# Optimization experiments

Hardware: AMD Instinct MI355X
Metric: run time of the kernel (lower is better)

## Reference

```python
import jax, jax.numpy as jnp
import numpy as np

D_MODEL = 1024
NHEAD = 16
HEAD_DIM = D_MODEL // NHEAD
EPS = 1e-8


def setup_inputs() -> dict:
    key = jax.random.key(0)
    ks = jax.random.split(key, 10)
    B, T = 2, 2048
    s = 1.0 / np.sqrt(D_MODEL)
    return {
        "query": jax.random.normal(ks[0], (B, T, D_MODEL), jnp.float32),
        "key": jax.random.normal(ks[1], (B, T, D_MODEL), jnp.float32),
        "value": jax.random.normal(ks[2], (B, T, D_MODEL), jnp.float32),
        "frac": jax.random.uniform(ks[3], (B, T), jnp.float32),
        "Wq": jax.random.normal(ks[4], (D_MODEL, D_MODEL), jnp.float32) * s,
        "bq": jnp.zeros((D_MODEL,), jnp.float32),
        "Wk": jax.random.normal(ks[5], (D_MODEL, D_MODEL), jnp.float32) * s,
        "bk": jnp.zeros((D_MODEL,), jnp.float32),
        "Wv": jax.random.normal(ks[6], (D_MODEL, D_MODEL), jnp.float32) * s,
        "bv": jnp.zeros((D_MODEL,), jnp.float32),
        "attn_bias": jax.random.normal(ks[7], (HEAD_DIM,), jnp.float32) * 0.02,
        "Wo": jax.random.normal(ks[8], (D_MODEL, D_MODEL), jnp.float32) * s,
        "bo": jnpp if False else jnp.zeros((D_MODEL,), jnp.float32),
    }


def reference(query, key, value, frac, Wq, bq, Wk, bk, Wv, bv, attn_bias, Wo, bo):
    B, T, _ = query.shape
    H, Dh = NHEAD, HEAD_DIM
    scale = Dh ** -0.5

    # torch Linear: x @ W.T + b
    Q = (query @ Wq.T + bq).reshape(B, T, H, Dh).transpose(0, 2, 1, 3)  # [B,H,T,Dh]
    K = (key @ Wk.T + bk).reshape(B, T, H, Dh).transpose(0, 2, 1, 3)
    V = (value @ Wv.T + bv).reshape(B, T, H, Dh).transpose(0, 2, 1, 3)

    # factor_ij = (frac_j - frac_i) / (frac_i*frac_j + eps), shape [B,T,T]
    fi = frac[:, :, None]
    fj = frac[:, None, :]
    factor = (fj - fi) / (fi * fj + EPS)

    # sum_d (Q_i*K_j + attn_bias*factor)_d == QK^T + sum(attn_bias)*factor
    bias_sum = jnp.sum(attn_bias)
    logits = jnp.einsum('bhid,bhjd->bhij', Q, K) + bias_sum * factor[:, None, :, :]
    logits = logits * scale

    probs = jax.nn.softmax(logits, axis=-1)  # dropout p=0.0 (eval)
    out = jnp.einsum('bhij,bhjd->bhid', probs, V)  # [B,H,T,Dh]
    out = out.transpose(0, 2, 1, 3).reshape(B, T, H * Dh)
    return out @ Wo.T + bo
```

## Files before the change

kernel.cpp:

```cpp
#include <hip/hip_runtime.h>

typedef short s16x8 __attribute__((ext_vector_type(8)));
typedef float f32x4 __attribute__((ext_vector_type(4)));
typedef unsigned int u32x2 __attribute__((ext_vector_type(2)));
typedef unsigned short u16;
typedef unsigned int u32;

#define D_MODEL 1024
#define NHEAD   16
#define HD      64
#define TSEQ    2048
#define NB      2
#define MROWS   4096
#define NSPLIT  2
#define NTILES  (TSEQ / 64 / NSPLIT)

#define LOG2E 1.4426950408889634f
#define QSCALE (0.125f * LOG2E)

__device__ __forceinline__ u16 f2bf(float f) {
  unsigned u = __builtin_bit_cast(unsigned, f);
  u += 0x7fffu + ((u >> 16) & 1u);
  return (u16)(u >> 16);
}

__device__ __forceinline__ float bf2f(u16 x) {
  return __builtin_bit_cast(float, (u32)x << 16);
}

__device__ __forceinline__ u32 cvtpk(float lo, float hi) {
  u32 r;
  asm("v_cvt_pk_bf16_f32 %0, %1, %2" : "=v"(r) : "v"(lo), "v"(hi));
  return r;
}

__device__ __forceinline__ float exp2fast(float x) {
#if __has_builtin(__builtin_amdgcn_exp2f)
  return __builtin_amdgcn_exp2f(x);
#else
  return exp2f(x);
#endif
}

__device__ __forceinline__ float rcpfast(float x) {
#if __has_builtin(__builtin_amdgcn_rcpf)
  return __builtin_amdgcn_rcpf(x);
#else
  return 1.f / x;
#endif
}

__device__ __forceinline__ void gload16(const void* g, void* l) {
  __builtin_amdgcn_global_load_lds((const __attribute__((address_space(1))) void*)g,
                                   (__attribute__((address_space(3))) void*)l,
                                   16, 0, 0);
}

__global__ void cvt_all(const float* __restrict__ q, const float* __restrict__ k,
                        const float* __restrict__ v, const float* __restrict__ wq,
                        const float* __restrict__ wk, const float* __restrict__ wv,
                        const float* __restrict__ wo, const float* __restrict__ ab,
                        u16* qb, u16* kb, u16* vb, u16* wqb, u16* wkb, u16* wvb, u16* wob,
                        float* bsum) {
  if (blockIdx.x == 16384) {
    if (threadIdx.x < 64) {
      float s = ab[threadIdx.x];
#pragma unroll
      for (int m = 32; m >= 1; m >>= 1) s += __shfl_xor(s, m);
      if (threadIdx.x == 0) bsum[0] = s * 0.125f * LOG2E;
    }
    return;
  }
  int i = blockIdx.x * 256 + threadIdx.x;
  const float* src; u16* dst; int off;
  if (i < 3 * 1048576) {
    int t = i >> 20; off = i & 1048575;
    src = (t == 0) ? q : (t == 1) ? k : v;
    dst = (t == 0) ? qb : (t == 1) ? kb : vb;
  } else {
    int j = i - 3 * 1048576;
    int t = j >> 18; off = j & 262143;
    src = (t == 0) ? wq : (t == 1) ? wk : (t == 2) ? wv : wo;
    dst = (t == 0) ? wqb : (t == 1) ? wkb : (t == 2) ? wvb : wob;
  }
  float4 x = ((const float4*)src)[off];
  ushort4 o;
  o.x = f2bf(x.x); o.y = f2bf(x.y); o.z = f2bf(x.z); o.w = f2bf(x.w);
  ((ushort4*)dst)[off] = o;
}

template <int BM, int BN, int WN, int MODE>
__device__ __forceinline__ void gemm_core(const u16* __restrict__ A, const u16* __restrict__ Bt,
                                          const float* __restrict__ bias, void* __restrict__ out,
                                          float oscale, u16* lds) {
  constexpr int K = 1024, N = 1024;
  constexpr int WM = 4 / WN;
  constexpr int WTM = BM / WM, WTN = BN / WN;
  constexpr int MR = WTM / 16, NR = WTN / 16;
  constexpr int ASZ = BM * 32, BSZ = BN * 32;
  constexpr int AISS = ASZ / 2048, BISS = BSZ / 2048;
  u16* lA = lds;
  u16* lB = lds + 2 * ASZ;

  const int tid = threadIdx.x;
  const int wid = tid >> 6, lane = tid & 63;
  const int l15 = lane & 15, lgp = lane >> 4;
  const int wr = wid / WN, wc = wid % WN;
  const int m0 = blockIdx.y * BM, n0 = blockIdx.x * BN;

  const u16* gA[AISS];
  const u16* gB[BISS];
#pragma unroll
  for (int i = 0; i < AISS; ++i) {
    int tp = i * 256 + tid, row = tp % BM, kc = tp / BM;
    gA[i] = A + (size_t)(m0 + row) * K + kc * 8;
  }
#pragma unroll
  for (int i = 0; i < BISS; ++i) {
    int tp = i * 256 + tid, row = tp % BN, kc = tp / BN;
    gB[i] = Bt + (size_t)(n0 + row) * K + kc * 8;
  }

  f32x4 acc[MR][NR];
#pragma unroll
  for (int m = 0; m < MR; ++m)
#pragma unroll
    for (int n = 0; n < NR; ++n) acc[m][n] = (f32x4){0.f, 0.f, 0.f, 0.f};

  auto stage = [&](int buf, int k0) {
#pragma unroll
    for (int i = 0; i < AISS; ++i)
      gload16(gA[i] + k0, lA + buf * ASZ + (i * 256 + tid) * 8);
#pragma unroll
    for (int i = 0; i < BISS; ++i)
      gload16(gB[i] + k0, lB + buf * BSZ + (i * 256 + tid) * 8);
  };

  int cur = 0;
  stage(0, 0);
  __syncthreads();
  for (int k0 = 0; k0 < K; k0 += 32) {
    if (k0 + 32 < K) stage(cur ^ 1, k0 + 32);
    const u16* a = lA + cur * ASZ;
    const u16* b = lB + cur * BSZ;
    s16x8 af[MR], bf[NR];
#pragma unroll
    for (int m = 0; m < MR; ++m)
      af[m] = *(const s16x8*)(a + lgp * BM * 8 + (wr * WTM + m * 16 + l15) * 8);
#pragma unroll
    for (int n = 0; n < NR; ++n)
      bf[n] = *(const s16x8*)(b + lgp * BN * 8 + (wc * WTN + n * 16 + l15) * 8);
    __builtin_amdgcn_s_setprio(1);
#pragma unroll
    for (int m = 0; m < MR; ++m)
#pragma unroll
      for (int n = 0; n < NR; ++n) {
        if (MODE == 1)
          acc[m][n] = __builtin_amdgcn_mfma_f32_16x16x32_bf16(bf[n], af[m], acc[m][n], 0, 0, 0);
        else
          acc[m][n] = __builtin_amdgcn_mfma_f32_16x16x32_bf16(af[m], bf[n], acc[m][n], 0, 0, 0);
      }
    __builtin_amdgcn_s_setprio(0);
    __syncthreads();
    cur ^= 1;
  }

  if (MODE == 1) {
    float4 bvv4[NR];
#pragma unroll
    for (int n = 0; n < NR; ++n)
      bvv4[n] = *(const float4*)(bias + n0 + wc * WTN + n * 16 + lgp * 4);
#pragma unroll
    for (int m = 0; m < MR; ++m) {
      int m_abs = m0 + wr * WTM + m * 16 + l15;
      int bb = m_abs >> 11, t = m_abs & 2047;
#pragma unroll
      for (int n = 0; n < NR; ++n) {
#pragma unroll
        for (int r = 0; r < 4; ++r) {
          int n_abs = n0 + wc * WTN + n * 16 + lgp * 4 + r;
          int h = n_abs >> 6, d = n_abs & 63;
          float vv = (acc[m][n][r] + ((const float*)&bvv4[n])[r]) * oscale;
          ((u16*)out)[(((size_t)((bb * NHEAD + h) * HD + d)) << 11) + t] = f2bf(vv);
        }
      }
    }
  } else {
    float bvv[NR];
#pragma unroll
    for (int n = 0; n < NR; ++n) bvv[n] = bias[n0 + wc * WTN + n * 16 + l15];
#pragma unroll
    for (int m = 0; m < MR; ++m) {
      int rowb = m0 + wr * WTM + m * 16 + lgp * 4;
#pragma unroll
      for (int n = 0; n < NR; ++n) {
        int col = n0 + wc * WTN + n * 16 + l15;
#pragma unroll
        for (int r = 0; r < 4; ++r) {
          int row = rowb + r;
          float vv = (acc[m][n][r] + bvv[n]) * oscale;
          if (MODE == 2) {
            ((float*)out)[(size_t)row * N + col] = vv;
          } else {
            int b = row >> 11, t = row & 2047;
            int h = col >> 6, d = col & 63;
            ((u16*)out)[(((size_t)(b * NHEAD + h) * TSEQ + t) << 6) + d] = f2bf(vv);
          }
        }
      }
    }
  }
}

__global__ __launch_bounds__(256) void gemm_qkv(const u16* __restrict__ qb, const u16* __restrict__ kb,
                                                const u16* __restrict__ vb,
                                                const u16* __restrict__ Wqb, const u16* __restrict__ Wkb,
                                                const u16* __restrict__ Wvb,
                                                const float* __restrict__ bq, const float* __restrict__ bk,
                                                const float* __restrict__ bv,
                                                u16* Qp, u16* Kp, u16* Vtp) {
  __shared__ __align__(16) u16 lds[2 * 128 * 32 * 2];
  int z = blockIdx.z;
  if (z == 0)
    gemm_core<128, 128, 2, 0>(qb, Wqb, bq, Qp, QSCALE, lds);
  else if (z == 1)
    gemm_core<128, 128, 2, 0>(kb, Wkb, bk, Kp, 1.0f, lds);
  else
    gemm_core<128, 128, 2, 1>(vb, Wvb, bv, Vtp, 1.0f, lds);
}

__global__ __launch_bounds__(256) void gemm_out(const u16* __restrict__ A, const u16* __restrict__ Bt,
                                                const float* __restrict__ bias, float* __restrict__ out) {
  __shared__ __align__(16) u16 lds[2 * 64 * 32 + 2 * 128 * 32];
  gemm_core<64, 128, 4, 2>(A, Bt, bias, out, 1.0f, lds);
}

__global__ __launch_bounds__(512, 4) void attn_kernel(const u16* __restrict__ Qp,
                                                      const u16* __restrict__ Kp,
                                                      const u16* __restrict__ Vt,
                                                      const float* __restrict__ frac,
                                                      const float* __restrict__ bsum,
                                                      u16* __restrict__ o0,
                                                      u16* __restrict__ o1,
                                                      float2* __restrict__ ml) {
  __shared__ __align__(16) u16 kbuf[64 * 64];
  __shared__ __align__(16) u16 vbuf[2][64 * 64];
  __shared__ __align__(16) u16 plds[8][16 * 64];
  const int tid = threadIdx.x, wid = tid >> 6, lane = tid & 63;
  const int l15 = lane & 15, lgp = lane >> 4;
  const int bh = blockIdx.y, b = bh >> 4, h = bh & 15;
  const int z = blockIdx.z;
  const int kvbase = z * (TSEQ / NSPLIT);
  u16* opart = z ? o1 : o0;
  float2* mlz = ml + z * (NB * NHEAD * TSEQ);
  const u16* Qh = Qp + (size_t)bh * TSEQ * HD;
  const u16* Kh = Kp + (size_t)bh * TSEQ * HD;
  const u16* Vh = Vt + (size_t)bh * HD * TSEQ;
  const float* fb = frac + b * TSEQ;
  const float bs = bsum[0];
  const float THR2 = 24.0f;
  const int q0 = blockIdx.x * 128 + wid * 16;

  const int srow = lane >> 3;
  const int sg8 = ((lane & 7) ^ srow) * 8;
  const int rbase = wid * 8 + srow;

  const int ofs0 = l15 * 64 + ((lgp ^ (l15 & 7)) * 8);
  const int ofs1 = l15 * 64 + (((4 + lgp) ^ (l15 & 7)) * 8);

  s16x8 qf[2];
#pragma unroll
  for (int ks = 0; ks < 2; ++ks)
    qf[ks] = *(const s16x8*)(Qh + (size_t)(q0 + l15) * HD + ks * 32 + lgp * 8);

  const float fi = fb[q0 + l15];
  const float nbfi = -bs * fi;
  float m2run = -1e30f;
  float lsum = 0.f;
  f32x4 o[4];
#pragma unroll
  for (int nd = 0; nd < 4; ++nd) o[nd] = (f32x4){0.f, 0.f, 0.f, 0.f};

  auto stageK = [&](int t) {
    int kv0s = kvbase + t * 64;
    gload16(Kh + (size_t)(kv0s + rbase) * HD + sg8, &kbuf[wid * 512]);
  };
  auto stageV = [&](int buf, int t) {
    int kv0s = kvbase + t * 64;
    gload16(Vh + (size_t)rbase * TSEQ + kv0s + sg8, &vbuf[buf][wid * 512]);
  };

  int cur = 0;
  stageK(0);
  stageV(0, 0);
  __syncthreads();

  for (int t = 0; t < NTILES; ++t) {
    s16x8 kf[4][2];
#pragma unroll
    for (int n = 0; n < 4; ++n) {
      kf[n][0] = *(const s16x8*)(&kbuf[0] + n * 1024 + ofs0);
      kf[n][1] = *(const s16x8*)(&kbuf[0] + n * 1024 + ofs1);
    }
    float4 fj4[4];
#pragma unroll
    for (int n = 0; n < 4; ++n)
      fj4[n] = *(const float4*)(fb + kvbase + t * 64 + n * 16 + lgp * 4);

    __syncthreads();
    if (t + 1 < NTILES) { stageK(t + 1); stageV(cur ^ 1, t + 1); }

    f32x4 s[4];
    __builtin_amdgcn_s_setprio(1);
#pragma unroll
    for (int n = 0; n < 4; ++n) {
      f32x4 a = (f32x4){0.f, 0.f, 0.f, 0.f};
      a = __builtin_amdgcn_mfma_f32_16x16x32_bf16(kf[n][0], qf[0], a, 0, 0, 0);
      a = __builtin_amdgcn_mfma_f32_16x16x32_bf16(kf[n][1], qf[1], a, 0, 0, 0);
      s[n] = a;
    }
    __builtin_amdgcn_s_setprio(0);

    float pmax = -1e30f;
#pragma unroll
    for (int n = 0; n < 4; ++n) {
#pragma unroll
      for (int r = 0; r < 4; ++r) {
        float fj = (r == 0) ? fj4[n].x : (r == 1) ? fj4[n].y : (r == 2) ? fj4[n].z : fj4[n].w;
        float num = __builtin_fmaf(bs, fj, nbfi);
        float den = __builtin_fmaf(fi, fj, 1e-8f);
        float l2 = __builtin_fmaf(num, rcpfast(den), s[n][r]);
        s[n][r] = l2;
        pmax = fmaxf(pmax, l2);
      }
    }

    if (__any((pmax - m2run) > THR2)) {
      float tm = fmaxf(pmax, __shfl_xor(pmax, 16));
      tm = fmaxf(tm, __shfl_xor(tm, 32));
      float m2n = fmaxf(m2run, tm);
      float alpha = exp2fast(m2run - m2n);
      lsum *= alpha;
      m2run = m2n;
      float af[4];
#pragma unroll
      for (int r = 0; r < 4; ++r) af[r] = __shfl(alpha, lgp * 4 + r);
#pragma unroll
      for (int nd = 0; nd < 4; ++nd)
#pragma unroll
        for (int r = 0; r < 4; ++r) o[nd][r] *= af[r];
    }

    u32 w[4][2];
    {
      float ps = 0.f;
#pragma unroll
      for (int n = 0; n < 4; ++n) {
#pragma unroll
        for (int s2 = 0; s2 < 2; ++s2) {
          float p0 = exp2fast(s[n][2 * s2 + 0] - m2run);
          float p1 = exp2fast(s[n][2 * s2 + 1] - m2run);
          ps += p0 + p1;
          w[n][s2] = cvtpk(p0, p1);
        }
      }
      lsum += ps;
    }

    u16* pw = &plds[wid][0];
#pragma unroll
    for (int n = 0; n < 4; ++n) {
      int idx = l15 * 64 + ((n * 16 + lgp * 4) ^ ((l15 & 7) << 3));
      *(u32x2*)(pw + idx) = (u32x2){w[n][0], w[n][1]};
    }
    s16x8 pf[2];
#pragma unroll
    for (int ks = 0; ks < 2; ++ks) {
      int idx = l15 * 64 + ((ks * 32 + lgp * 8) ^ ((l15 & 7) << 3));
      pf[ks] = *(const s16x8*)(pw + idx);
    }

    const u16* vbp = &vbuf[cur][0];
    __builtin_amdgcn_s_setprio(1);
#pragma unroll
    for (int nd = 0; nd < 4; ++nd) {
      s16x8 vf0 = *(const s16x8*)(vbp + nd * 1024 + ofs0);
      s16x8 vf1 = *(const s16x8*)(vbp + nd * 1024 + ofs1);
      o[nd] = __builtin_amdgcn_mfma_f32_16x16x32_bf16(pf[0], vf0, o[nd], 0, 0, 0);
      o[nd] = __builtin_amdgcn_mfma_f32_16x16x32_bf16(pf[1], vf1, o[nd], 0, 0, 0);
    }
    __builtin_amdgcn_s_setprio(0);

    __syncthreads();
    cur ^= 1;
  }

  {
    float l = lsum;
    l += __shfl_xor(l, 16);
    l += __shfl_xor(l, 32);
    if (lgp == 0)
      mlz[(bh << 11) + q0 + l15] = make_float2(m2run, l);
#pragma unroll
    for (int nd = 0; nd < 4; ++nd)
#pragma unroll
      for (int r = 0; r < 4; ++r) {
        int q = q0 + lgp * 4 + r;
        opart[((size_t)(b * TSEQ + q)) * D_MODEL + h * HD + nd * 16 + l15] = f2bf(o[nd][r]);
      }
  }
}

__global__ __launch_bounds__(256) void attn_combine(const u16* __restrict__ o0,
                                                    const u16* __restrict__ o1,
                                                    const float2* __restrict__ ml,
                                                    u16* __restrict__ aout) {
  int g = blockIdx.x * 256 + threadIdx.x;
  int bth = g >> 3, j0 = (g & 7) * 8;
  int b = bth >> 15, t = (bth >> 4) & 2047, h = bth & 15;
  int mlidx = (((b << 4) | h) << 11) | t;
  float2 v0 = ml[mlidx];
  float2 v1 = ml[NB * NHEAD * TSEQ + mlidx];
  float M = fmaxf(v0.x, v1.x);
  float a0 = exp2fast(v0.x - M), a1 = exp2fast(v1.x - M);
  float rd = __fdividef(1.f, __builtin_fmaf(v0.y, a0, v1.y * a1));
  float s0 = a0 * rd, s1 = a1 * rd;
  size_t base = (size_t)bth * 64 + j0;
  s16x8 x0 = *(const s16x8*)(o0 + base);
  s16x8 x1 = *(const s16x8*)(o1 + base);
  s16x8 out;
#pragma unroll
  for (int j = 0; j < 8; ++j) {
    float f = __builtin_fmaf(bf2f((u16)x0[j]), s0, bf2f((u16)x1[j]) * s1);
    out[j] = (short)f2bf(f);
  }
  *(s16x8*)(aout + base) = out;
}

extern "C" void kernel_launch(void* const* d_in, const int* in_sizes, int n_in,
                              void* d_out, int out_size, void* d_ws, size_t ws_size,
                              hipStream_t stream) {
  const float* query = (const float*)d_in[0];
  const float* key_  = (const float*)d_in[1];
  const float* value = (const float*)d_in[2];
  const float* frac  = (const float*)d_in[3];
  const float* Wq    = (const float*)d_in[4];
  const float* bq    = (const float*)d_in[5];
  const float* Wk    = (const float*)d_in[6];
  const float* bk    = (const float*)d_in[7];
  const float* Wv    = (const float*)d_in[8];
  const float* bv    = (const float*)d_in[9];
  const float* abias = (const float*)d_in[10];
  const float* Wo    = (const float*)d_in[11];
  const float* bo    = (const float*)d_in[12];

  char* ws = (char*)d_ws;
  size_t off = 0;
  auto alloc = [&](size_t bytes) { char* p = ws + off; off += (bytes + 255) & ~255ULL; return p; };
  const size_t XB = (size_t)MROWS * D_MODEL * 2;
  const size_t WB = (size_t)D_MODEL * D_MODEL * 2;
  u16* qb  = (u16*)alloc(XB);
  u16* kb  = (u16*)alloc(XB);
  u16* vb  = (u16*)alloc(XB);
  u16* Wqb = (u16*)alloc(WB);
  u16* Wkb = (u16*)alloc(WB);
  u16* Wvb = (u16*)alloc(WB);
  u16* Wob = (u16*)alloc(WB);
  float* bsum = (float*)alloc(256);
  u16* Qp  = (u16*)alloc(XB);
  u16* Kp  = (u16*)alloc(XB);
  u16* Vtp = (u16*)alloc(XB);
  u16* AO  = (u16*)alloc(XB);

  u16* o0 = qb;
  u16* o1 = kb;
  float2* ml = (float2*)vb;

  cvt_all<<<dim3(16385), dim3(256), 0, stream>>>(query, key_, value, Wq, Wk, Wv, Wo, abias,
                                                 qb, kb, vb, Wqb, Wkb, Wvb, Wob, bsum);

  gemm_qkv<<<dim3(D_MODEL / 128, MROWS / 128, 3), dim3(256), 0, stream>>>(
      qb, kb, vb, Wqb, Wkb, Wvb, bq, bk, bv, Qp, Kp, Vtp);

  attn_kernel<<<dim3(TSEQ / 128, NB * NHEAD, NSPLIT), dim3(512), 0, stream>>>(
      Qp, Kp, Vtp, frac, bsum, o0, o1, ml);

  attn_combine<<<dim3(MROWS * D_MODEL / 8 / 256), dim3(256), 0, stream>>>(o0, o1, ml, AO);

  gemm_out<<<dim3(D_MODEL / 128, MROWS / 64), dim3(256), 0, stream>>>(AO, Wob, bo, (float*)d_out);
}
```

Measured before the change: 182.3 us.

## Switch attention to 32x32x16 MFMA with register-only P via permlane32 swap

The attention kernel moves from 16x16x32 to 32x32x16 bf16 MFMA tiles, with each wave owning 32 query rows. The block shrinks from 512 to 256 threads and each thread now stages two K and two V chunks. The softmax probability tile is rearranged into the B-operand layout in registers using v_permlane32_swap instead of a per-wave LDS round trip. The aims are fewer MFMA issues, no P store/load through LDS, and fewer shuffles for the running-max rescale, at the cost of more accumulator registers per lane and halved threads per block.

```diff
diff --git a/kernel.cpp b/kernel.cpp
--- a/kernel.cpp
+++ b/kernel.cpp
@@ -2,7 +2,9 @@
 
 typedef short s16x8 __attribute__((ext_vector_type(8)));
 typedef float f32x4 __attribute__((ext_vector_type(4)));
+typedef float f32x16 __attribute__((ext_vector_type(16)));
 typedef unsigned int u32x2 __attribute__((ext_vector_type(2)));
+typedef unsigned int u32x4 __attribute__((ext_vector_type(4)));
 typedef unsigned short u16;
 typedef unsigned int u32;
 
@@ -235,7 +237,7 @@
   gemm_core<64, 128, 4, 2>(A, Bt, bias, out, 1.0f, lds);
 }
 
-__global__ __launch_bounds__(512, 4) void attn_kernel(const u16* __restrict__ Qp,
+__global__ __launch_bounds__(256, 4) void attn_kernel(const u16* __restrict__ Qp,
                                                       const u16* __restrict__ Kp,
                                                       const u16* __restrict__ Vt,
                                                       const float* __restrict__ frac,
@@ -245,9 +247,9 @@
                                                       float2* __restrict__ ml) {
   __shared__ __align__(16) u16 kbuf[64 * 64];
   __shared__ __align__(16) u16 vbuf[2][64 * 64];
-  __shared__ __align__(16) u16 plds[8][16 * 64];
   const int tid = threadIdx.x, wid = tid >> 6, lane = tid & 63;
-  const int l15 = lane & 15, lgp = lane >> 4;
+  const int l31 = lane & 31, hi = lane >> 5, hi4 = hi * 4, hi8 = hi * 8;
+  const int ksw = l31 & 7;
   const int bh = blockIdx.y, b = bh >> 4, h = bh & 15;
   const int z = blockIdx.z;
   const int kvbase = z * (TSEQ / NSPLIT);
@@ -259,135 +261,129 @@
   const float* fb = frac + b * TSEQ;
   const float bs = bsum[0];
   const float THR2 = 24.0f;
-  const int q0 = blockIdx.x * 128 + wid * 16;
-
-  const int srow = lane >> 3;
-  const int sg8 = ((lane & 7) ^ srow) * 8;
-  const int rbase = wid * 8 + srow;
-
-  const int ofs0 = l15 * 64 + ((lgp ^ (l15 & 7)) * 8);
-  const int ofs1 = l15 * 64 + (((4 + lgp) ^ (l15 & 7)) * 8);
-
-  s16x8 qf[2];
-#pragma unroll
-  for (int ks = 0; ks < 2; ++ks)
-    qf[ks] = *(const s16x8*)(Qh + (size_t)(q0 + l15) * HD + ks * 32 + lgp * 8);
-
-  const float fi = fb[q0 + l15];
+  const int q0w = blockIdx.x * 128 + wid * 32;
+
+  const int r_0 = tid >> 3, c_0 = ((tid & 7) ^ (r_0 & 7)) * 8;
+  const int r_1 = 32 + r_0, c_1 = ((tid & 7) ^ (r_1 & 7)) * 8;
+  const u16* Ksrc0 = Kh + (size_t)r_0 * HD + c_0;
+  const u16* Ksrc1 = Kh + (size_t)r_1 * HD + c_1;
+  const u16* Vsrc0 = Vh + (size_t)r_0 * TSEQ + c_0;
+  const u16* Vsrc1 = Vh + (size_t)r_1 * TSEQ + c_1;
+  u16* kdst0 = &kbuf[(wid * 64) * 8];
+  u16* kdst1 = &kbuf[(256 + wid * 64) * 8];
+
+  s16x8 qf[4];
+#pragma unroll
+  for (int dc = 0; dc < 4; ++dc)
+    qf[dc] = *(const s16x8*)(Qh + (size_t)(q0w + l31) * HD + dc * 16 + hi8);
+
+  const float fi = fb[q0w + l31];
   const float nbfi = -bs * fi;
-  float m2run = -1e30f;
-  float lsum = 0.f;
-  f32x4 o[4];
-#pragma unroll
-  for (int nd = 0; nd < 4; ++nd) o[nd] = (f32x4){0.f, 0.f, 0.f, 0.f};
-
-  auto stageK = [&](int t) {
+  float m2run = -1e30f, lsum = 0.f;
+  f32x16 o2[2];
+#pragma unroll
+  for (int dh = 0; dh < 2; ++dh)
+#pragma unroll
+    for (int i = 0; i < 16; ++i) o2[dh][i] = 0.f;
+
+  auto stage = [&](int buf, int t) {
     int kv0s = kvbase + t * 64;
-    gload16(Kh + (size_t)(kv0s + rbase) * HD + sg8, &kbuf[wid * 512]);
+    gload16(Ksrc0 + (size_t)kv0s * HD, kdst0);
+    gload16(Ksrc1 + (size_t)kv0s * HD, kdst1);
+    gload16(Vsrc0 + kv0s, &vbuf[buf][(wid * 64) * 8]);
+    gload16(Vsrc1 + kv0s, &vbuf[buf][(256 + wid * 64) * 8]);
   };
-  auto stageV = [&](int buf, int t) {
-    int kv0s = kvbase + t * 64;
-    gload16(Vh + (size_t)rbase * TSEQ + kv0s + sg8, &vbuf[buf][wid * 512]);
-  };
 
   int cur = 0;
-  stageK(0);
-  stageV(0, 0);
+  stage(0, 0);
   __syncthreads();
 
   for (int t = 0; t < NTILES; ++t) {
-    s16x8 kf[4][2];
-#pragma unroll
-    for (int n = 0; n < 4; ++n) {
-      kf[n][0] = *(const s16x8*)(&kbuf[0] + n * 1024 + ofs0);
-      kf[n][1] = *(const s16x8*)(&kbuf[0] + n * 1024 + ofs1);
-    }
-    float4 fj4[4];
-#pragma unroll
-    for (int n = 0; n < 4; ++n)
-      fj4[n] = *(const float4*)(fb + kvbase + t * 64 + n * 16 + lgp * 4);
+    const int kvt = kvbase + t * 64;
+
+    f32x16 s2[2];
+    __builtin_amdgcn_s_setprio(1);
+#pragma unroll
+    for (int t2 = 0; t2 < 2; ++t2) {
+      f32x16 a;
+#pragma unroll
+      for (int i = 0; i < 16; ++i) a[i] = 0.f;
+#pragma unroll
+      for (int dc = 0; dc < 4; ++dc) {
+        s16x8 kf = *(const s16x8*)(&kbuf[(t2 * 32 + l31) * 64 + (((dc * 2 + hi) ^ ksw) * 8)]);
+        a = __builtin_amdgcn_mfma_f32_32x32x16_bf16(kf, qf[dc], a, 0, 0, 0);
+      }
+      s2[t2] = a;
+    }
+    __builtin_amdgcn_s_setprio(0);
 
     __syncthreads();
-    if (t + 1 < NTILES) { stageK(t + 1); stageV(cur ^ 1, t + 1); }
-
-    f32x4 s[4];
-    __builtin_amdgcn_s_setprio(1);
-#pragma unroll
-    for (int n = 0; n < 4; ++n) {
-      f32x4 a = (f32x4){0.f, 0.f, 0.f, 0.f};
-      a = __builtin_amdgcn_mfma_f32_16x16x32_bf16(kf[n][0], qf[0], a, 0, 0, 0);
-      a = __builtin_amdgcn_mfma_f32_16x16x32_bf16(kf[n][1], qf[1], a, 0, 0, 0);
-      s[n] = a;
-    }
-    __builtin_amdgcn_s_setprio(0);
+    if (t + 1 < NTILES) stage(cur ^ 1, t + 1);
 
     float pmax = -1e30f;
 #pragma unroll
-    for (int n = 0; n < 4; ++n) {
-#pragma unroll
-      for (int r = 0; r < 4; ++r) {
-        float fj = (r == 0) ? fj4[n].x : (r == 1) ? fj4[n].y : (r == 2) ? fj4[n].z : fj4[n].w;
-        float num = __builtin_fmaf(bs, fj, nbfi);
-        float den = __builtin_fmaf(fi, fj, 1e-8f);
-        float l2 = __builtin_fmaf(num, rcpfast(den), s[n][r]);
-        s[n][r] = l2;
-        pmax = fmaxf(pmax, l2);
+    for (int t2 = 0; t2 < 2; ++t2) {
+#pragma unroll
+      for (int g = 0; g < 4; ++g) {
+        float4 fj4 = *(const float4*)(fb + kvt + t2 * 32 + g * 8 + hi4);
+#pragma unroll
+        for (int r4 = 0; r4 < 4; ++r4) {
+          float fjv = (r4 == 0) ? fj4.x : (r4 == 1) ? fj4.y : (r4 == 2) ? fj4.z : fj4.w;
+          float num = __builtin_fmaf(bs, fjv, nbfi);
+          float den = __builtin_fmaf(fi, fjv, 1e-8f);
+          float l2 = __builtin_fmaf(num, rcpfast(den), s2[t2][g * 4 + r4]);
+          s2[t2][g * 4 + r4] = l2;
+          pmax = fmaxf(pmax, l2);
+        }
       }
     }
 
     if (__any((pmax - m2run) > THR2)) {
-      float tm = fmaxf(pmax, __shfl_xor(pmax, 16));
-      tm = fmaxf(tm, __shfl_xor(tm, 32));
+      float tm = fmaxf(pmax, __shfl_xor(pmax, 32));
       float m2n = fmaxf(m2run, tm);
       float alpha = exp2fast(m2run - m2n);
       lsum *= alpha;
       m2run = m2n;
-      float af[4];
-#pragma unroll
-      for (int r = 0; r < 4; ++r) af[r] = __shfl(alpha, lgp * 4 + r);
-#pragma unroll
-      for (int nd = 0; nd < 4; ++nd)
-#pragma unroll
-        for (int r = 0; r < 4; ++r) o[nd][r] *= af[r];
-    }
-
-    u32 w[4][2];
-    {
-      float ps = 0.f;
-#pragma unroll
-      for (int n = 0; n < 4; ++n) {
-#pragma unroll
-        for (int s2 = 0; s2 < 2; ++s2) {
-          float p0 = exp2fast(s[n][2 * s2 + 0] - m2run);
-          float p1 = exp2fast(s[n][2 * s2 + 1] - m2run);
-          ps += p0 + p1;
-          w[n][s2] = cvtpk(p0, p1);
-        }
-      }
-      lsum += ps;
-    }
-
-    u16* pw = &plds[wid][0];
-#pragma unroll
-    for (int n = 0; n < 4; ++n) {
-      int idx = l15 * 64 + ((n * 16 + lgp * 4) ^ ((l15 & 7) << 3));
-      *(u32x2*)(pw + idx) = (u32x2){w[n][0], w[n][1]};
-    }
-    s16x8 pf[2];
-#pragma unroll
-    for (int ks = 0; ks < 2; ++ks) {
-      int idx = l15 * 64 + ((ks * 32 + lgp * 8) ^ ((l15 & 7) << 3));
-      pf[ks] = *(const s16x8*)(pw + idx);
+#pragma unroll
+      for (int reg = 0; reg < 16; ++reg) {
+        float av = __shfl(alpha, (reg & 3) + 8 * (reg >> 2) + hi4);
+        o2[0][reg] *= av;
+        o2[1][reg] *= av;
+      }
+    }
+
+    s16x8 pa[4];
+#pragma unroll
+    for (int t2 = 0; t2 < 2; ++t2) {
+      u32 uu[8];
+#pragma unroll
+      for (int k = 0; k < 8; ++k) {
+        float p0 = exp2fast(s2[t2][2 * k + 0] - m2run);
+        float p1 = exp2fast(s2[t2][2 * k + 1] - m2run);
+        lsum += p0 + p1;
+        uu[k] = cvtpk(p0, p1);
+      }
+      u32 a0 = uu[0], b0 = uu[2];
+      asm("v_permlane32_swap_b32 %0, %1" : "+v"(a0), "+v"(b0));
+      u32 a1 = uu[1], b1 = uu[3];
+      asm("v_permlane32_swap_b32 %0, %1" : "+v"(a1), "+v"(b1));
+      pa[t2 * 2] = __builtin_bit_cast(s16x8, (u32x4){a0, a1, b0, b1});
+      u32 a2 = uu[4], b2 = uu[6];
+      asm("v_permlane32_swap_b32 %0, %1" : "+v"(a2), "+v"(b2));
+      u32 a3 = uu[5], b3 = uu[7];
+      asm("v_permlane32_swap_b32 %0, %1" : "+v"(a3), "+v"(b3));
+      pa[t2 * 2 + 1] = __builtin_bit_cast(s16x8, (u32x4){a2, a3, b2, b3});
     }
 
     const u16* vbp = &vbuf[cur][0];
     __builtin_amdgcn_s_setprio(1);
 #pragma unroll
-    for (int nd = 0; nd < 4; ++nd) {
-      s16x8 vf0 = *(const s16x8*)(vbp + nd * 1024 + ofs0);
-      s16x8 vf1 = *(const s16x8*)(vbp + nd * 1024 + ofs1);
-      o[nd] = __builtin_amdgcn_mfma_f32_16x16x32_bf16(pf[0], vf0, o[nd], 0, 0, 0);
-      o[nd] = __builtin_amdgcn_mfma_f32_16x16x32_bf16(pf[1], vf1, o[nd], 0, 0, 0);
+    for (int dh = 0; dh < 2; ++dh) {
+#pragma unroll
+      for (int ks = 0; ks < 4; ++ks) {
+        s16x8 vf = *(const s16x8*)(vbp + (dh * 32 + l31) * 64 + (((ks * 2 + hi) ^ ksw) * 8));
+        o2[dh] = __builtin_amdgcn_mfma_f32_32x32x16_bf16(pa[ks], vf, o2[dh], 0, 0, 0);
+      }
     }
     __builtin_amdgcn_s_setprio(0);
 
@@ -395,20 +391,16 @@
     cur ^= 1;
   }
 
-  {
-    float l = lsum;
-    l += __shfl_xor(l, 16);
-    l += __shfl_xor(l, 32);
-    if (lgp == 0)
-      mlz[(bh << 11) + q0 + l15] = make_float2(m2run, l);
-#pragma unroll
-    for (int nd = 0; nd < 4; ++nd)
-#pragma unroll
-      for (int r = 0; r < 4; ++r) {
-        int q = q0 + lgp * 4 + r;
-        opart[((size_t)(b * TSEQ + q)) * D_MODEL + h * HD + nd * 16 + l15] = f2bf(o[nd][r]);
-      }
-  }
+  lsum += __shfl_xor(lsum, 32);
+  if (hi == 0)
+    mlz[(bh << 11) + q0w + l31] = make_float2(m2run, lsum);
+#pragma unroll
+  for (int dh = 0; dh < 2; ++dh)
+#pragma unroll
+    for (int reg = 0; reg < 16; ++reg) {
+      int q = q0w + (reg & 3) + 8 * (reg >> 2) + hi4;
+      opart[((size_t)(b * TSEQ + q)) * D_MODEL + h * HD + dh * 32 + l31] = f2bf(o2[dh][reg]);
+    }
 }
 
 __global__ __launch_bounds__(256) void attn_combine(const u16* __restrict__ o0,
@@ -482,7 +474,7 @@
   gemm_qkv<<<dim3(D_MODEL / 128, MROWS / 128, 3), dim3(256), 0, stream>>>(
       qb, kb, vb, Wqb, Wkb, Wvb, bq, bk, bv, Qp, Kp, Vtp);
 
-  attn_kernel<<<dim3(TSEQ / 128, NB * NHEAD, NSPLIT), dim3(512), 0, stream>>>(
+  attn_kernel<<<dim3(TSEQ / 128, NB * NHEAD, NSPLIT), dim3(256), 0, stream>>>(
       Qp, Kp, Vtp, frac, bsum, o0, o1, ml);
 
   attn_combine<<<dim3(MROWS * D_MODEL / 8 / 256), dim3(256), 0, stream>>>(o0, o1, ml, AO);
```

Measured after the change: 181.7 us. About the same (-0.3%).
